# Optimization experiments

Measured on AMD Instinct MI355X. Metric: run time of the kernel, lower is better.

Reference implementation:

```python
import jax, jax.numpy as jnp
import numpy as np

# ---- config (matches init_kwargs) ----
C_IN, C_OUT = 320, 320
KH, KW = 3, 3
STRIDE, PAD = 1, 1
RANK = 32
IN_FEAT = 2944   # 320*9=2880 padded to multiple of 128
OUT_FEAT = 384   # 320 padded to multiple of 128
QMAX = 7.0       # symmetric int4: clip to [-8, 7], scale = amax/7


def unfold_nchw(x, kh, kw, stride, pad):
    # torch F.unfold ordering: features flattened as (C, kh, kw), channel-major
    N, C, H, W = x.shape
    xp = jnp.pad(x, ((0, 0), (0, 0), (pad, pad), (pad, pad)))
    Ho = (H + 2 * pad - kh) // stride + 1
    Wo = (W + 2 * pad - kw) // stride + 1
    patches = [xp[:, :, i:i + stride * Ho:stride, j:j + stride * Wo:stride]
               for i in range(kh) for j in range(kw)]
    p = jnp.stack(patches, axis=2)              # (N, C, kh*kw, Ho, Wo)
    return p.reshape(N, C * kh * kw, Ho * Wo)   # (N, C*kh*kw, L)


def quant_int4(t, axis):
    s = jnp.maximum(jnp.max(jnp.abs(t), axis=axis, keepdims=True) / QMAX, 1e-8)
    q = jnp.clip(jnp.round(t / s), -8.0, 7.0)
    return q, s


def setup_inputs() -> dict:
    key = jax.random.key(0)
    k1, k2, k3, k4, k5 = jax.random.split(key, 5)
    x = jax.random.normal(k1, (4, C_IN, 64, 64), dtype=jnp.float32)
    w = jax.random.normal(k2, (OUT_FEAT, IN_FEAT), dtype=jnp.float32) * 0.02
    proj_down = jax.random.normal(k3, (IN_FEAT, RANK), dtype=jnp.float32) * 0.02
    proj_up = jax.random.normal(k4, (RANK, OUT_FEAT), dtype=jnp.float32) * 0.02
    bias = jax.random.normal(k5, (OUT_FEAT,), dtype=jnp.float32) * 0.01
    return {"x": x, "w": w, "proj_down": proj_down, "proj_up": proj_up, "bias": bias}


def reference(x, w, proj_down, proj_up, bias):
    # im2col unfold -> (N, L, C*kh*kw)
    xu = unfold_nchw(x, KH, KW, STRIDE, PAD).transpose(0, 2, 1)
    # zero-pad feature dim to padded in_features
    xu = jnp.pad(xu, ((0, 0), (0, 0), (0, IN_FEAT - xu.shape[2])))
    # SVD low-rank branch (full precision)
    y_lora = jnp.einsum('nlr,ro->nlo', jnp.einsum('nlk,kr->nlr', xu, proj_down), proj_up)
    # W4A4 quantized branch: per-token act scales, per-out-channel weight scales
    qx, sx = quant_int4(xu, axis=2)          # (N,L,K), (N,L,1)
    qw, sw = quant_int4(w, axis=1)           # (O,K), (O,1)
    y_q = jnp.einsum('nlk,ok->nlo', qx, qw) * sx * sw[:, 0]
    return y_q + y_lora + bias
```

## Files before the change

kernel.cpp:

```cpp
#include <hip/hip_runtime.h>
#include <hip/hip_fp16.h>
#include <hip/hip_bf16.h>
#include <stdint.h>
#include <stddef.h>

#define C_INC 320
#define KREAL 2880
#define KPAD  2944
#define OUT_F 384
#define RANK  32
#define HH    64
#define WW    64
#define NTOK  16384
#define NCH   16
#define CCH   20
#define QSTR  76

typedef int   vi4 __attribute__((ext_vector_type(4)));
typedef float v4f __attribute__((ext_vector_type(4)));
typedef short s8v __attribute__((ext_vector_type(8)));

static __device__ __forceinline__ void async16(const void* g, void* l) {
    __builtin_amdgcn_global_load_lds(
        (const __attribute__((address_space(1))) unsigned int*)g,
        (__attribute__((address_space(3))) unsigned int*)l, 16, 0, 0);
}

static __device__ __forceinline__ unsigned short f2bf(float f) {
    __hip_bfloat16 h = __float2bfloat16(f);
    union { __hip_bfloat16 h; unsigned short u; } c; c.h = h; return c.u;
}

__global__ __launch_bounds__(256) void kq_w(const float* __restrict__ w,
                                            int8_t* __restrict__ qw,
                                            float* __restrict__ sw) {
    int o = blockIdx.x;
    const float* row = w + (size_t)o * KPAD;
    float m = 0.f;
    for (int k = threadIdx.x; k < KPAD; k += 256) m = fmaxf(m, fabsf(row[k]));
    #pragma unroll
    for (int off = 32; off > 0; off >>= 1) m = fmaxf(m, __shfl_down(m, off, 64));
    __shared__ float red[4];
    __shared__ float sval;
    if ((threadIdx.x & 63) == 0) red[threadIdx.x >> 6] = m;
    __syncthreads();
    if (threadIdx.x == 0) {
        float mm = fmaxf(fmaxf(red[0], red[1]), fmaxf(red[2], red[3]));
        sval = fmaxf(mm / 7.0f, 1e-8f);
        sw[o] = sval;
    }
    __syncthreads();
    float s = sval;
    for (int k = threadIdx.x; k < KPAD; k += 256) {
        float q = rintf(row[k] / s);
        q = fminf(fmaxf(q, -8.f), 7.f);
        qw[(size_t)o * KPAD + k] = (int8_t)q;
    }
}

__global__ __launch_bounds__(256) void k_chmax(const float* __restrict__ x,
                                               float* __restrict__ mb2) {
    int p = blockIdx.x * 256 + threadIdx.x;
    int cc = blockIdx.y;
    int n = p >> 12, hw = p & 4095;
    const float* base = x + ((size_t)(n * C_INC) + cc * 40) * 4096 + hw;
    float m = 0.f;
    #pragma unroll 4
    for (int c = 0; c < 40; ++c) m = fmaxf(m, fabsf(base[(size_t)c * 4096]));
    mb2[(size_t)cc * NTOK + p] = m;
}

__global__ __launch_bounds__(256) void k_sx(const float* __restrict__ mb2,
                                            float* __restrict__ sx) {
    int p = blockIdx.x * 256 + threadIdx.x;
    int n = p >> 12, hw = p & 4095;
    int h = hw >> 6, w = hw & 63;
    float m = 0.f;
    #pragma unroll
    for (int cc = 0; cc < 8; ++cc) {
        const float* pl = mb2 + (size_t)cc * NTOK + (n << 12);
        #pragma unroll
        for (int di = -1; di <= 1; ++di)
            #pragma unroll
            for (int dj = -1; dj <= 1; ++dj) {
                int hh = h + di, ww = w + dj;
                if ((unsigned)hh < (unsigned)HH && (unsigned)ww < (unsigned)WW)
                    m = fmaxf(m, pl[(hh << 6) + ww]);
            }
    }
    sx[p] = fmaxf(m / 7.0f, 1e-8f);
}

__global__ __launch_bounds__(256) void k_im2q(const float* __restrict__ x,
                                              const float* __restrict__ sx,
                                              int8_t* __restrict__ qx) {
    __shared__ int8_t qbuf[256 * QSTR];
    const int pstart[4] = {0, 8, 16, 20};
    const int phoff[3]  = {0, 72, 144};

    int tid = threadIdx.x;
    int rg = blockIdx.x;
    int cc = blockIdx.y;
    int n = rg >> 4, h4 = rg & 15;
    int wid = tid >> 6, lane = tid & 63;
    int ha = h4 * 4 + wid;
    int c0 = cc * CCH;

    int ta = (n << 12) + (ha << 6) + lane;
    float inva = 1.0f / sx[ta];
    const float* xrowa = x + ((size_t)(n * C_INC) + c0) * 4096 + (ha << 6) + lane;
    bool hok0a = (ha > 0), hok2a = (ha < 63);
    bool wok0 = (lane > 0), wok2 = (lane < 63);
    int bt = (n << 12) + (h4 << 8);
    int qra = tid;

    for (int ph = 0; ph < 3; ++ph) {
        int ps = pstart[ph], pch = pstart[ph + 1] - ps;
        __syncthreads();
        if (ph > 0) {
            for (int i = tid; i < 256 * 18; i += 256) {
                int row = i / 18, col = i - row * 18;
                *(unsigned int*)&qx[(size_t)(bt + row) * KPAD + cc * 180 + phoff[ph - 1] + col * 4] =
                    *(unsigned int*)&qbuf[row * QSTR + col * 4];
            }
        }
        __syncthreads();

        const float* xca = xrowa + (size_t)ps * 4096;
        float r0a = hok0a ? xca[-64] : 0.f, r1a = xca[0], r2a = hok2a ? xca[64] : 0.f;

        for (int cl = 0; cl < pch; ++cl) {
            float p0a = 0.f, p1a = 0.f, p2a = 0.f;
            if (cl + 1 < pch) {
                const float* xna = xrowa + (size_t)(ps + cl + 1) * 4096;
                p0a = hok0a ? xna[-64] : 0.f; p1a = xna[0]; p2a = hok2a ? xna[64] : 0.f;
            }
            float va[9];
            {
                float u0 = __shfl_up(r0a, 1, 64), d0 = __shfl_down(r0a, 1, 64);
                float u1 = __shfl_up(r1a, 1, 64), d1 = __shfl_down(r1a, 1, 64);
                float u2 = __shfl_up(r2a, 1, 64), d2 = __shfl_down(r2a, 1, 64);
                va[0] = wok0 ? u0 : 0.f; va[1] = r0a; va[2] = wok2 ? d0 : 0.f;
                va[3] = wok0 ? u1 : 0.f; va[4] = r1a; va[5] = wok2 ? d1 : 0.f;
                va[6] = wok0 ? u2 : 0.f; va[7] = r2a; va[8] = wok2 ? d2 : 0.f;
            }
            #pragma unroll
            for (int u = 0; u < 9; ++u) {
                float qa = rintf(va[u] * inva);
                qa = fminf(fmaxf(qa, -8.f), 7.f);
                qbuf[qra * QSTR + cl * 9 + u] = (int8_t)qa;
            }
            r0a = p0a; r1a = p1a; r2a = p2a;
        }
    }

    __syncthreads();
    if (cc == NCH - 1) {
        for (int i = tid; i < 256 * 25; i += 256) {
            int row = i / 25, col = i - row * 25;
            unsigned int vdw = (col < 9) ? *(unsigned int*)&qbuf[row * QSTR + col * 4] : 0u;
            *(unsigned int*)&qx[(size_t)(bt + row) * KPAD + cc * 180 + 144 + col * 4] = vdw;
        }
    } else {
        for (int i = tid; i < 256 * 9; i += 256) {
            int row = i / 9, col = i - row * 9;
            *(unsigned int*)&qx[(size_t)(bt + row) * KPAD + cc * 180 + 144 + col * 4] =
                *(unsigned int*)&qbuf[row * QSTR + col * 4];
        }
    }
}

__global__ __launch_bounds__(256) void k_down(const float* __restrict__ x,
                                              const float* __restrict__ pd,
                                              __half* __restrict__ Sh) {
    __shared__ unsigned short Abuf[144 * 168];
    int tid = threadIdx.x;
    int mhalf = blockIdx.x;
    int nb = blockIdx.y;
    int w = tid >> 6, lane = tid & 63;
    int lg = lane >> 4, lr = lane & 15;
    int n = nb >> 5;
    int hw0 = (nb & 31) * 128 + w * 32;
    const float* xn = x + (size_t)n * (C_INC * 4096);

    v4f acc[9][2];
    #pragma unroll
    for (int mt = 0; mt < 9; ++mt) { acc[mt][0] = (v4f)0.f; acc[mt][1] = (v4f)0.f; }

    for (int p = 0; p < 2; ++p) {
        __syncthreads();
        for (int i = tid; i < 160 * 144; i += 256) {
            int cl = i / 144, ml = i - cl * 144;
            int c = p * 160 + cl;
            float v = pd[(size_t)c * 288 + mhalf * 144 + ml];
            Abuf[ml * 168 + cl] = f2bf(v);
        }
        __syncthreads();

        #pragma unroll
        for (int ksl = 0; ksl < 5; ++ksl) {
            const float* bp0 = xn + (size_t)(p * 160 + ksl * 32 + lg * 8) * 4096 + hw0 + lr;
            const float* bp1 = bp0 + 16;
            s8v b0, b1;
            #pragma unroll
            for (int e = 0; e < 8; ++e) {
                b0[e] = (short)f2bf(bp0[(size_t)e * 4096]);
                b1[e] = (short)f2bf(bp1[(size_t)e * 4096]);
            }
            #pragma unroll
            for (int mt = 0; mt < 9; ++mt) {
                s8v a = *(s8v*)&Abuf[(mt * 16 + lr) * 168 + ksl * 32 + lg * 8];
                acc[mt][0] = __builtin_amdgcn_mfma_f32_16x16x32_bf16(a, b0, acc[mt][0], 0, 0, 0);
                acc[mt][1] = __builtin_amdgcn_mfma_f32_16x16x32_bf16(a, b1, acc[mt][1], 0, 0, 0);
            }
        }
    }

    int colbase = (n << 12) + hw0 + lr;
    #pragma unroll
    for (int mt = 0; mt < 9; ++mt)
        #pragma unroll
        for (int nt = 0; nt < 2; ++nt)
            #pragma unroll
            for (int r = 0; r < 4; ++r) {
                int row = mhalf * 144 + mt * 16 + lg * 4 + r;
                Sh[(size_t)row * NTOK + colbase + nt * 16] = __float2half_rn(acc[mt][nt][r]);
            }
}

__global__ __launch_bounds__(256) void k_gemm(const int8_t* __restrict__ qx,
                                              const int8_t* __restrict__ qw,
                                              const float* __restrict__ sx,
                                              const float* __restrict__ sw,
                                              float* __restrict__ out) {
    __shared__ int8_t lsA[2][64 * 64];
    __shared__ int8_t lsB[2][128 * 64];
    int tid = threadIdx.x;
    int n0 = blockIdx.x * 128;
    int m0 = blockIdx.y * 64;
    int wid = tid >> 6, lane = tid & 63;
    int wr = wid >> 1, wc = wid & 1;
    int lg = lane >> 4, lr = lane & 15;

    const int8_t* gA  = qx + (size_t)(m0 + wid * 16 + (lane >> 2)) * KPAD + (lane & 3) * 16;
    const int8_t* gB0 = qw + (size_t)(n0 + wid * 16 + (lane >> 2)) * KPAD + (lane & 3) * 16;
    const int8_t* gB1 = gB0 + (size_t)64 * KPAD;
    int lofs = wid * 1024;

    vi4 acc[2][4];
    #pragma unroll
    for (int i = 0; i < 2; ++i)
        #pragma unroll
        for (int j = 0; j < 4; ++j) acc[i][j] = (vi4)0;

    async16(gA, &lsA[0][lofs]);
    async16(gB0, &lsB[0][lofs]);
    async16(gB1, &lsB[0][4096 + lofs]);
    __syncthreads();

    int cur = 0;
    for (int kk = 64; kk < KPAD; kk += 64) {
        int nxt = cur ^ 1;
        async16(gA + kk, &lsA[nxt][lofs]);
        async16(gB0 + kk, &lsB[nxt][lofs]);
        async16(gB1 + kk, &lsB[nxt][4096 + lofs]);
        vi4 af[2], bf[4];
        #pragma unroll
        for (int mi = 0; mi < 2; ++mi)
            af[mi] = *(vi4*)&lsA[cur][(wr * 32 + mi * 16 + lr) * 64 + lg * 16];
        #pragma unroll
        for (int ni = 0; ni < 4; ++ni)
            bf[ni] = *(vi4*)&lsB[cur][(wc * 64 + ni * 16 + lr) * 64 + lg * 16];
        #pragma unroll
        for (int mi = 0; mi < 2; ++mi)
            #pragma unroll
            for (int ni = 0; ni < 4; ++ni)
                acc[mi][ni] = __builtin_amdgcn_mfma_i32_16x16x64_i8(af[mi], bf[ni], acc[mi][ni], 0, 0, 0);
        __syncthreads();
        cur = nxt;
    }
    {
        vi4 af[2], bf[4];
        #pragma unroll
        for (int mi = 0; mi < 2; ++mi)
            af[mi] = *(vi4*)&lsA[cur][(wr * 32 + mi * 16 + lr) * 64 + lg * 16];
        #pragma unroll
        for (int ni = 0; ni < 4; ++ni)
            bf[ni] = *(vi4*)&lsB[cur][(wc * 64 + ni * 16 + lr) * 64 + lg * 16];
        #pragma unroll
        for (int mi = 0; mi < 2; ++mi)
            #pragma unroll
            for (int ni = 0; ni < 4; ++ni)
                acc[mi][ni] = __builtin_amdgcn_mfma_i32_16x16x64_i8(af[mi], bf[ni], acc[mi][ni], 0, 0, 0);
    }

    float swv[4];
    #pragma unroll
    for (int ni = 0; ni < 4; ++ni) swv[ni] = sw[n0 + wc * 64 + ni * 16 + lr];
    #pragma unroll
    for (int mi = 0; mi < 2; ++mi) {
        int rbase = m0 + wr * 32 + mi * 16 + lg * 4;
        #pragma unroll
        for (int r = 0; r < 4; ++r) {
            int row = rbase + r;
            float sxv = sx[row];
            #pragma unroll
            for (int ni = 0; ni < 4; ++ni) {
                int col = n0 + wc * 64 + ni * 16 + lr;
                out[(size_t)row * OUT_F + col] = ((float)acc[mi][ni][r] * sxv) * swv[ni];
            }
        }
    }
}

__global__ __launch_bounds__(384) void k_epi(float* __restrict__ out,
                                             const __half* __restrict__ Sh,
                                             const float* __restrict__ up,
                                             const float* __restrict__ bias) {
    __shared__ float rs[32][RANK];
    int tid = threadIdx.x;
    int o = tid;
    float uc[RANK];
    #pragma unroll
    for (int j = 0; j < RANK; ++j) uc[j] = up[(size_t)j * OUT_F + o];
    float b = bias[o];
    int t0 = blockIdx.x * 32;
    for (int i = tid; i < 32 * RANK; i += 384) {
        int tt = i & 31, j = i >> 5;
        int t = t0 + tt;
        int n12 = t & ~4095;
        int hw = t & 4095, h = hw >> 6, w = hw & 63;
        float s = 0.f;
        #pragma unroll
        for (int u = 0; u < 9; ++u) {
            int hh = h + u / 3 - 1, wv = w + u % 3 - 1;
            if ((unsigned)hh < (unsigned)HH && (unsigned)wv < (unsigned)WW)
                s += __half2float(Sh[(size_t)(u * 32 + j) * NTOK + n12 + (hh << 6) + wv]);
        }
        rs[tt][j] = s;
    }
    __syncthreads();
    for (int tt = 0; tt < 32; ++tt) {
        int t = t0 + tt;
        float a = out[(size_t)t * OUT_F + o];
        float l = 0.f;
        const v4f* rv = (const v4f*)&rs[tt][0];
        #pragma unroll
        for (int j4 = 0; j4 < 8; ++j4) {
            v4f r4 = rv[j4];
            l = fmaf(r4[0], uc[4 * j4 + 0], l);
            l = fmaf(r4[1], uc[4 * j4 + 1], l);
            l = fmaf(r4[2], uc[4 * j4 + 2], l);
            l = fmaf(r4[3], uc[4 * j4 + 3], l);
        }
        out[(size_t)t * OUT_F + o] = a + l + b;
    }
}

extern "C" void kernel_launch(void* const* d_in, const int* in_sizes, int n_in,
                              void* d_out, int out_size, void* d_ws, size_t ws_size,
                              hipStream_t stream) {
    const float* x    = (const float*)d_in[0];
    const float* w    = (const float*)d_in[1];
    const float* pd   = (const float*)d_in[2];
    const float* pu   = (const float*)d_in[3];
    const float* bias = (const float*)d_in[4];
    float* out = (float*)d_out;

    char* ws = (char*)d_ws;
    int8_t* qw    = (int8_t*)(ws + 0);
    float*  sw    = (float*) (ws + 1130496);
    float*  mb2   = (float*) (ws + 1132032);
    float*  sx    = (float*) (ws + 1656320);
    int8_t* qx    = (int8_t*)(ws + 1721856);
    __half* Sh    = (__half*)(ws + 49956352);

    hipLaunchKernelGGL(kq_w,    dim3(OUT_F),    dim3(256), 0, stream, w, qw, sw);
    hipLaunchKernelGGL(k_chmax, dim3(64, 8),    dim3(256), 0, stream, x, mb2);
    hipLaunchKernelGGL(k_sx,    dim3(64),       dim3(256), 0, stream, mb2, sx);
    hipLaunchKernelGGL(k_im2q,  dim3(64, NCH),  dim3(256), 0, stream, x, sx, qx);
    hipLaunchKernelGGL(k_down,  dim3(2, 128),   dim3(256), 0, stream, x, pd, Sh);
    hipLaunchKernelGGL(k_gemm,  dim3(3, 256),   dim3(256), 0, stream, qx, qw, sx, sw, out);
    hipLaunchKernelGGL(k_epi,   dim3(512),      dim3(384), 0, stream, out, Sh, pu, bias);
}
```

Baseline: 222.5 us.

## Double GEMM K-tile to 128 and XOR-swizzle LDS layout

```diff
diff --git a/kernel.cpp b/kernel.cpp
--- a/kernel.cpp
+++ b/kernel.cpp
@@ -15,6 +15,7 @@
 #define NCH   16
 #define CCH   20
 #define QSTR  76
+#define BK    128
 
 typedef int   vi4 __attribute__((ext_vector_type(4)));
 typedef float v4f __attribute__((ext_vector_type(4)));
@@ -233,8 +234,8 @@
                                               const float* __restrict__ sx,
                                               const float* __restrict__ sw,
                                               float* __restrict__ out) {
-    __shared__ int8_t lsA[2][64 * 64];
-    __shared__ int8_t lsB[2][128 * 64];
+    __shared__ int8_t lsA[2][64 * BK];
+    __shared__ int8_t lsB[2][128 * BK];
     int tid = threadIdx.x;
     int n0 = blockIdx.x * 128;
     int m0 = blockIdx.y * 64;
@@ -242,10 +243,10 @@
     int wr = wid >> 1, wc = wid & 1;
     int lg = lane >> 4, lr = lane & 15;
 
-    const int8_t* gA  = qx + (size_t)(m0 + wid * 16 + (lane >> 2)) * KPAD + (lane & 3) * 16;
-    const int8_t* gB0 = qw + (size_t)(n0 + wid * 16 + (lane >> 2)) * KPAD + (lane & 3) * 16;
-    const int8_t* gB1 = gB0 + (size_t)64 * KPAD;
-    int lofs = wid * 1024;
+    int srow = lane >> 3;
+    int sslot = (lane & 7) ^ srow;
+    const int8_t* gA = qx + (size_t)m0 * KPAD;
+    const int8_t* gB = qw + (size_t)n0 * KPAD;
 
     vi4 acc[2][4];
     #pragma unroll
@@ -253,40 +254,66 @@
         #pragma unroll
         for (int j = 0; j < 4; ++j) acc[i][j] = (vi4)0;
 
-    async16(gA, &lsA[0][lofs]);
-    async16(gB0, &lsB[0][lofs]);
-    async16(gB1, &lsB[0][4096 + lofs]);
+    #pragma unroll
+    for (int i = 0; i < 2; ++i) {
+        int c = wid + i * 4;
+        async16(gA + (size_t)(c * 8 + srow) * KPAD + sslot * 16, &lsA[0][c * 1024]);
+    }
+    #pragma unroll
+    for (int i = 0; i < 4; ++i) {
+        int c = wid + i * 4;
+        async16(gB + (size_t)(c * 8 + srow) * KPAD + sslot * 16, &lsB[0][c * 1024]);
+    }
     __syncthreads();
 
     int cur = 0;
-    for (int kk = 64; kk < KPAD; kk += 64) {
+    for (int kk = BK; kk < KPAD; kk += BK) {
         int nxt = cur ^ 1;
-        async16(gA + kk, &lsA[nxt][lofs]);
-        async16(gB0 + kk, &lsB[nxt][lofs]);
-        async16(gB1 + kk, &lsB[nxt][4096 + lofs]);
-        vi4 af[2], bf[4];
-        #pragma unroll
-        for (int mi = 0; mi < 2; ++mi)
-            af[mi] = *(vi4*)&lsA[cur][(wr * 32 + mi * 16 + lr) * 64 + lg * 16];
-        #pragma unroll
-        for (int ni = 0; ni < 4; ++ni)
-            bf[ni] = *(vi4*)&lsB[cur][(wc * 64 + ni * 16 + lr) * 64 + lg * 16];
-        #pragma unroll
-        for (int mi = 0; mi < 2; ++mi)
-            #pragma unroll
-            for (int ni = 0; ni < 4; ++ni)
-                acc[mi][ni] = __builtin_amdgcn_mfma_i32_16x16x64_i8(af[mi], bf[ni], acc[mi][ni], 0, 0, 0);
+        #pragma unroll
+        for (int i = 0; i < 2; ++i) {
+            int c = wid + i * 4;
+            async16(gA + (size_t)(c * 8 + srow) * KPAD + kk + sslot * 16, &lsA[nxt][c * 1024]);
+        }
+        #pragma unroll
+        for (int i = 0; i < 4; ++i) {
+            int c = wid + i * 4;
+            async16(gB + (size_t)(c * 8 + srow) * KPAD + kk + sslot * 16, &lsB[nxt][c * 1024]);
+        }
+        #pragma unroll
+        for (int k2 = 0; k2 < 2; ++k2) {
+            vi4 af[2], bf[4];
+            #pragma unroll
+            for (int mi = 0; mi < 2; ++mi) {
+                int row = wr * 32 + mi * 16 + lr;
+                af[mi] = *(vi4*)&lsA[cur][row * BK + (((k2 * 4 + lg) ^ (lr & 7)) << 4)];
+            }
+            #pragma unroll
+            for (int ni = 0; ni < 4; ++ni) {
+                int row = wc * 64 + ni * 16 + lr;
+                bf[ni] = *(vi4*)&lsB[cur][row * BK + (((k2 * 4 + lg) ^ (lr & 7)) << 4)];
+            }
+            #pragma unroll
+            for (int mi = 0; mi < 2; ++mi)
+                #pragma unroll
+                for (int ni = 0; ni < 4; ++ni)
+                    acc[mi][ni] = __builtin_amdgcn_mfma_i32_16x16x64_i8(af[mi], bf[ni], acc[mi][ni], 0, 0, 0);
+        }
         __syncthreads();
         cur = nxt;
     }
-    {
+    #pragma unroll
+    for (int k2 = 0; k2 < 2; ++k2) {
         vi4 af[2], bf[4];
         #pragma unroll
-        for (int mi = 0; mi < 2; ++mi)
-            af[mi] = *(vi4*)&lsA[cur][(wr * 32 + mi * 16 + lr) * 64 + lg * 16];
-        #pragma unroll
-        for (int ni = 0; ni < 4; ++ni)
-            bf[ni] = *(vi4*)&lsB[cur][(wc * 64 + ni * 16 + lr) * 64 + lg * 16];
+        for (int mi = 0; mi < 2; ++mi) {
+            int row = wr * 32 + mi * 16 + lr;
+            af[mi] = *(vi4*)&lsA[cur][row * BK + (((k2 * 4 + lg) ^ (lr & 7)) << 4)];
+        }
+        #pragma unroll
+        for (int ni = 0; ni < 4; ++ni) {
+            int row = wc * 64 + ni * 16 + lr;
+            bf[ni] = *(vi4*)&lsB[cur][row * BK + (((k2 * 4 + lg) ^ (lr & 7)) << 4)];
+        }
         #pragma unroll
         for (int mi = 0; mi < 2; ++mi)
             #pragma unroll
```

After: 213.1 us. 1.04x faster.
